# Performance work log

Measured on AMD Instinct MI355X. Metric: run time of the kernel, lower is better.

## Reference

```python
import jax, jax.numpy as jnp
import numpy as np

BATCH, LATENT_DIM, NUM_QUBITS = 32768, 2048, 24


def setup_inputs() -> dict:
    key = jax.random.key(0)
    k1, k2, k3, k4 = jax.random.split(key, 4)
    return {
        "latent": jax.random.normal(k1, (BATCH, LATENT_DIM), dtype=jnp.float32),
        "W": jax.random.normal(k2, (NUM_QUBITS, LATENT_DIM), dtype=jnp.float32) * (1.0 / np.sqrt(LATENT_DIM)),
        "b": jax.random.normal(k3, (NUM_QUBITS,), dtype=jnp.float32) * 0.01,
        "params": jax.random.normal(k4, (NUM_QUBITS, 3), dtype=jnp.float32),
    }


def reference(latent, W, b, params):
    # Classical projection: (B, L) @ (L, Q) + (Q,) -> per-qubit encoding angle a
    a = jnp.einsum("bl,ql->bq", latent, W) + b  # (B, Q)
    # Circuit per qubit: RY(a) on |0>, then Rot(phi, theta, omega) = RZ(omega)RY(theta)RZ(phi).
    # Bloch vector after RY(a): (sin a, 0, cos a). RZ(phi) then RY(theta) give
    # z = cos(a)cos(theta) - sin(a)cos(phi)sin(theta); final RZ(omega) leaves <Z> unchanged.
    phi = params[:, 0]    # (Q,)
    theta = params[:, 1]  # (Q,)
    return jnp.cos(a) * jnp.cos(theta) - jnp.sin(a) * (jnp.cos(phi) * jnp.sin(theta))
```

## Files before the change

kernel.cpp:

```cpp
#include <hip/hip_runtime.h>
#include <cstdint>


#define NQ 24
#define LDIM 2048
#define BATCH 32768
#define NKT 64

typedef __attribute__((ext_vector_type(8))) short bf16x8;
typedef __attribute__((ext_vector_type(4))) float f32x4;

union U4 { uint4 u; bf16x8 s; };

__device__ __forceinline__ uint cvt_pk_bf16(float lo, float hi) {
    uint r;
    asm("v_cvt_pk_bf16_f32 %0, %1, %2" : "=v"(r) : "v"(lo), "v"(hi));
    return r;
}

struct Stage { float4 a0, a1; uint4 b0, b1; };

__device__ __forceinline__ void issue(Stage& s, const float* ap, const uint4* bp, int t) {
    s.a0 = *(const float4*)(ap + t * 32);
    s.a1 = *(const float4*)(ap + t * 32 + 4);
    s.b0 = bp[t * 128];
    s.b1 = bp[t * 128 + 64];
}

__device__ __forceinline__ void computeS(const Stage& s, f32x4& c0, f32x4& c1) {
    uint h0 = cvt_pk_bf16(s.a0.x, s.a0.y);
    uint h1 = cvt_pk_bf16(s.a0.z, s.a0.w);
    uint h2 = cvt_pk_bf16(s.a1.x, s.a1.y);
    uint h3 = cvt_pk_bf16(s.a1.z, s.a1.w);
    float r0 = __uint_as_float(h0 << 16), r1 = __uint_as_float(h0 & 0xFFFF0000u);
    float r2 = __uint_as_float(h1 << 16), r3 = __uint_as_float(h1 & 0xFFFF0000u);
    float r4 = __uint_as_float(h2 << 16), r5 = __uint_as_float(h2 & 0xFFFF0000u);
    float r6 = __uint_as_float(h3 << 16), r7 = __uint_as_float(h3 & 0xFFFF0000u);
    uint l0 = cvt_pk_bf16(s.a0.x - r0, s.a0.y - r1);
    uint l1 = cvt_pk_bf16(s.a0.z - r2, s.a0.w - r3);
    uint l2 = cvt_pk_bf16(s.a1.x - r4, s.a1.y - r5);
    uint l3 = cvt_pk_bf16(s.a1.z - r6, s.a1.w - r7);
    U4 ah, al, b0, b1;
    ah.u = make_uint4(h0, h1, h2, h3);
    al.u = make_uint4(l0, l1, l2, l3);
    b0.u = s.b0;
    b1.u = s.b1;
    c0 = __builtin_amdgcn_mfma_f32_16x16x32_bf16(ah.s, b0.s, c0, 0, 0, 0);
    c1 = __builtin_amdgcn_mfma_f32_16x16x32_bf16(ah.s, b1.s, c1, 0, 0, 0);
    c0 = __builtin_amdgcn_mfma_f32_16x16x32_bf16(al.s, b0.s, c0, 0, 0, 0);
    c1 = __builtin_amdgcn_mfma_f32_16x16x32_bf16(al.s, b1.s, c1, 0, 0, 0);
}

__global__ __launch_bounds__(256, 2) void qll_main(
    const float* __restrict__ latent,
    const uint4* __restrict__ wb,
    const float* __restrict__ bvec,
    const float* __restrict__ ctv,
    const float* __restrict__ csv,
    float* __restrict__ out)
{
    const int tid  = threadIdx.x;
    const int wave = tid >> 6;
    const int lane = tid & 63;
    const int mrow = lane & 15;
    const int kgrp = lane >> 4;
    const int row0 = (blockIdx.x * 4 + wave) * 16;

    const float* ap = latent + (size_t)(row0 + mrow) * LDIM + kgrp * 8;
    const uint4* bp = wb + lane;

    f32x4 c0 = {0.f, 0.f, 0.f, 0.f};
    f32x4 c1 = {0.f, 0.f, 0.f, 0.f};

    Stage S0, S1, S2;
    issue(S0, ap, bp, 0);
    issue(S1, ap, bp, 1);
    issue(S2, ap, bp, 2);

    #pragma unroll 1
    for (int t = 0; t <= NKT - 7; t += 3) {
        computeS(S0, c0, c1); issue(S0, ap, bp, t + 3);
        computeS(S1, c0, c1); issue(S1, ap, bp, t + 4);
        computeS(S2, c0, c1); issue(S2, ap, bp, t + 5);
    }
    computeS(S0, c0, c1); issue(S0, ap, bp, 63);
    computeS(S1, c0, c1);
    computeS(S2, c0, c1);
    computeS(S0, c0, c1);

    #pragma unroll
    for (int qt = 0; qt < 2; qt++) {
        const int q = qt * 16 + mrow;
        const bool valid = (q < NQ);
        const float bv = valid ? bvec[q] : 0.f;
        const float ct = valid ? ctv[q]  : 0.f;
        const float cs = valid ? csv[q]  : 0.f;
        const f32x4 c = qt ? c1 : c0;
        #pragma unroll
        for (int r = 0; r < 4; r++) {
            const int row = row0 + kgrp * 4 + r;
            const float a = c[r] + bv;
            float s, co;
            __sincosf(a, &s, &co);
            if (valid) out[(size_t)row * NQ + q] = co * ct - s * cs;
        }
    }
}

__global__ __launch_bounds__(256) void qll_prep(
    const float* __restrict__ W, const float* __restrict__ params,
    ushort* __restrict__ wb, float* __restrict__ ctcs)
{
    const int idx = blockIdx.x * 256 + threadIdx.x;
    const int kt  = idx >> 10;
    const int rem = idx & 1023;
    const int qt  = rem >> 9;
    const int l   = (rem >> 3) & 63;
    const int e   = rem & 7;
    const int q   = qt * 16 + (l & 15);
    const int k   = kt * 32 + (l >> 4) * 8 + e;
    float v = (q < NQ) ? W[q * LDIM + k] : 0.f;
    uint u = __float_as_uint(v);
    wb[idx] = (ushort)((u + 0x7FFF + ((u >> 16) & 1)) >> 16);
    if (idx < NQ) {
        float phi = params[3 * idx + 0];
        float th  = params[3 * idx + 1];
        ctcs[idx]      = cosf(th);
        ctcs[NQ + idx] = cosf(phi) * sinf(th);
    }
}

extern "C" void kernel_launch(void* const* d_in, const int* in_sizes, int n_in,
                              void* d_out, int out_size, void* d_ws, size_t ws_size,
                              hipStream_t stream) {
    (void)in_sizes; (void)n_in; (void)out_size; (void)ws_size;
    const float* latent = (const float*)d_in[0];
    const float* W      = (const float*)d_in[1];
    const float* bvec   = (const float*)d_in[2];
    const float* params = (const float*)d_in[3];
    float* out  = (float*)d_out;
    ushort* wb  = (ushort*)d_ws;
    float* ctcs = (float*)d_ws + 32768;

    hipLaunchKernelGGL(qll_prep, dim3(256), dim3(256), 0, stream,
                       W, params, wb, ctcs);
    hipLaunchKernelGGL(qll_main, dim3(BATCH / 64), dim3(256), 0, stream,
                       latent, (const uint4*)wb, bvec, ctcs, ctcs + NQ, out);
}
```

Measured before the change: 52.88 us.

## Split K dimension across wave pairs with LDS reduction and deeper pipeline

Each 16-row tile is now processed by two waves, each covering half of the reduction dimension. Their partial accumulators are summed through shared memory before the sincos epilogue. The grid doubles, launch bounds ask for higher occupancy, and the prefetch pipeline goes from three to four stages to keep more loads in flight on a bandwidth-bound GEMV-like workload. The cost is a block-wide barrier, an LDS round trip, and an epilogue where half the waves sit idle.

```diff
diff --git a/kernel.cpp b/kernel.cpp
--- a/kernel.cpp
+++ b/kernel.cpp
@@ -5,7 +5,7 @@
 #define NQ 24
 #define LDIM 2048
 #define BATCH 32768
-#define NKT 64
+#define NT 32
 
 typedef __attribute__((ext_vector_type(8))) short bf16x8;
 typedef __attribute__((ext_vector_type(4))) float f32x4;
@@ -51,7 +51,7 @@
     c1 = __builtin_amdgcn_mfma_f32_16x16x32_bf16(al.s, b1.s, c1, 0, 0, 0);
 }
 
-__global__ __launch_bounds__(256, 2) void qll_main(
+__global__ __launch_bounds__(256, 4) void qll_main(
     const float* __restrict__ latent,
     const uint4* __restrict__ wb,
     const float* __restrict__ bvec,
@@ -59,50 +59,71 @@
     const float* __restrict__ csv,
     float* __restrict__ out)
 {
-    const int tid  = threadIdx.x;
-    const int wave = tid >> 6;
-    const int lane = tid & 63;
-    const int mrow = lane & 15;
-    const int kgrp = lane >> 4;
-    const int row0 = (blockIdx.x * 4 + wave) * 16;
+    __shared__ float lred[2][8][64];
 
-    const float* ap = latent + (size_t)(row0 + mrow) * LDIM + kgrp * 8;
-    const uint4* bp = wb + lane;
+    const int tid   = threadIdx.x;
+    const int wave  = tid >> 6;
+    const int lane  = tid & 63;
+    const int khalf = wave & 1;
+    const int rtile = wave >> 1;
+    const int mrow  = lane & 15;
+    const int kgrp  = lane >> 4;
+    const int row0  = (blockIdx.x * 2 + rtile) * 16;
+
+    const float* ap = latent + (size_t)(row0 + mrow) * LDIM + khalf * (NT * 32) + kgrp * 8;
+    const uint4* bp = wb + (size_t)khalf * NT * 128 + lane;
 
     f32x4 c0 = {0.f, 0.f, 0.f, 0.f};
     f32x4 c1 = {0.f, 0.f, 0.f, 0.f};
 
-    Stage S0, S1, S2;
+    Stage S0, S1, S2, S3;
     issue(S0, ap, bp, 0);
     issue(S1, ap, bp, 1);
     issue(S2, ap, bp, 2);
+    issue(S3, ap, bp, 3);
 
     #pragma unroll 1
-    for (int t = 0; t <= NKT - 7; t += 3) {
-        computeS(S0, c0, c1); issue(S0, ap, bp, t + 3);
-        computeS(S1, c0, c1); issue(S1, ap, bp, t + 4);
-        computeS(S2, c0, c1); issue(S2, ap, bp, t + 5);
+    for (int t = 0; t <= NT - 8; t += 4) {
+        computeS(S0, c0, c1); issue(S0, ap, bp, t + 4);
+        computeS(S1, c0, c1); issue(S1, ap, bp, t + 5);
+        computeS(S2, c0, c1); issue(S2, ap, bp, t + 6);
+        computeS(S3, c0, c1); issue(S3, ap, bp, t + 7);
     }
-    computeS(S0, c0, c1); issue(S0, ap, bp, 63);
+    computeS(S0, c0, c1);
     computeS(S1, c0, c1);
     computeS(S2, c0, c1);
-    computeS(S0, c0, c1);
+    computeS(S3, c0, c1);
 
-    #pragma unroll
-    for (int qt = 0; qt < 2; qt++) {
-        const int q = qt * 16 + mrow;
-        const bool valid = (q < NQ);
-        const float bv = valid ? bvec[q] : 0.f;
-        const float ct = valid ? ctv[q]  : 0.f;
-        const float cs = valid ? csv[q]  : 0.f;
-        const f32x4 c = qt ? c1 : c0;
+    if (khalf) {
         #pragma unroll
-        for (int r = 0; r < 4; r++) {
-            const int row = row0 + kgrp * 4 + r;
-            const float a = c[r] + bv;
-            float s, co;
-            __sincosf(a, &s, &co);
-            if (valid) out[(size_t)row * NQ + q] = co * ct - s * cs;
+        for (int j = 0; j < 4; j++) {
+            lred[rtile][j][lane]     = c0[j];
+            lred[rtile][4 + j][lane] = c1[j];
+        }
+    }
+    __syncthreads();
+    if (!khalf) {
+        #pragma unroll
+        for (int j = 0; j < 4; j++) {
+            c0[j] += lred[rtile][j][lane];
+            c1[j] += lred[rtile][4 + j][lane];
+        }
+        #pragma unroll
+        for (int qt = 0; qt < 2; qt++) {
+            const int q = qt * 16 + mrow;
+            const bool valid = (q < NQ);
+            const float bv = valid ? bvec[q] : 0.f;
+            const float ct = valid ? ctv[q]  : 0.f;
+            const float cs = valid ? csv[q]  : 0.f;
+            const f32x4 c = qt ? c1 : c0;
+            #pragma unroll
+            for (int r = 0; r < 4; r++) {
+                const int row = row0 + kgrp * 4 + r;
+                const float a = c[r] + bv;
+                float s, co;
+                __sincosf(a, &s, &co);
+                if (valid) out[(size_t)row * NQ + q] = co * ct - s * cs;
+            }
         }
     }
 }
@@ -144,6 +165,6 @@
 
     hipLaunchKernelGGL(qll_prep, dim3(256), dim3(256), 0, stream,
                        W, params, wb, ctcs);
-    hipLaunchKernelGGL(qll_main, dim3(BATCH / 64), dim3(256), 0, stream,
+    hipLaunchKernelGGL(qll_main, dim3(BATCH / 32), dim3(256), 0, stream,
                        latent, (const uint4*)wb, bvec, ctcs, ctcs + NQ, out);
 }
```

Result: slower. 56.23 us (+6.3%).
